# Performance work log

Hardware: AMD Instinct MI355X
Metric: run time of the kernel (lower is better)

## Reference

```python
import jax, jax.numpy as jnp
import numpy as np

K = 10  # knn_graph default neighbors (self excluded)
NEG = 0.2  # LeakyReLU slope


def lrelu(x):
    return jnp.where(x > 0, x, NEG * x)


def conv1x1_1d(x, w):  # x: (B,Ci,N), w: (Co,Ci)
    return jnp.einsum('oi,bin->bon', w, x)


def conv1x1_2d(x, w):  # x: (B,Ci,N,k), w: (Co,Ci)
    return jnp.einsum('oi,bink->bonk', w, x)


def bn1(x, s, b):  # folded eval-mode BN, x: (B,C,N)
    return x * s[None, :, None] + b[None, :, None]


def bn2(x, s, b):  # x: (B,C,N,k)
    return x * s[None, :, None, None] + b[None, :, None, None]


def knn_graph(x, k=K):
    # x: (B, D, N) -> edge features (B, 2D, N, k)
    xt = jnp.transpose(x, (0, 2, 1))  # (B,N,D)
    sq = jnp.sum(xt * xt, axis=-1)  # (B,N)
    d2 = sq[:, :, None] + sq[:, None, :] - 2.0 * jnp.einsum('bnd,bmd->bnm', xt, xt)
    _, idx = jax.lax.top_k(-d2, k + 1)  # nearest k+1 incl. self
    idx = idx[:, :, 1:]  # drop self -> (B,N,k)
    B = xt.shape[0]
    feats = xt[jnp.arange(B)[:, None, None], idx]  # (B,N,k,D)
    center = xt[:, :, None, :]  # (B,N,1,D)
    edge = jnp.concatenate((feats - center, jnp.broadcast_to(center, feats.shape)), axis=-1)
    return jnp.transpose(edge, (0, 3, 1, 2))  # (B,2D,N,k)


def _make_params(key):
    ks = iter(jax.random.split(key, 32))
    def W(co, ci):
        return jax.random.normal(next(ks), (co, ci), jnp.float32) * (1.0 / np.sqrt(ci))
    def SB(c):
        return (jax.random.uniform(next(ks), (c,), jnp.float32, 0.5, 1.5),
                jax.random.normal(next(ks), (c,), jnp.float32) * 0.1)
    p = {}
    p['w1'] = W(64, 6);    p['s1'], p['b1'] = SB(64)
    p['w2'] = W(64, 64);   p['s2'], p['b2'] = SB(64)
    p['w3'] = W(64, 128);  p['s3'], p['b3'] = SB(64)
    p['w4'] = W(64, 64);   p['s4'], p['b4'] = SB(64)
    p['w5'] = W(64, 128);  p['s5'], p['b5'] = SB(64)
    p['w6'] = W(1024, 192); p['s6'], p['b6'] = SB(1024)
    p['w7'] = W(64, 16);   p['s7'], p['b7'] = SB(64)
    p['wp1'] = W(256, 1280); p['sp1'], p['bp1'] = SB(256)
    p['wp2'] = W(256, 256);  p['sp2'], p['bp2'] = SB(256)
    p['wp3'] = W(128, 256);  p['sp3'], p['bp3'] = SB(128)
    p['wp4'] = W(6, 128)
    return p


def setup_inputs() -> dict:
    key = jax.random.key(0)
    k0, k1, k2 = jax.random.split(key, 3)
    inp = {
        'points': jax.random.normal(k0, (8, 2048, 3), jnp.float32),
        'label': jax.random.uniform(k1, (8, 16), jnp.float32),
    }
    inp.update(_make_params(k2))
    return inp


def reference(points, label,
              w1, s1, b1, w2, s2, b2, w3, s3, b3, w4, s4, b4, w5, s5, b5,
              w6, s6, b6, w7, s7, b7,
              wp1, sp1, bp1, wp2, sp2, bp2, wp3, sp3, bp3, wp4):
    B, N, _ = points.shape
    x0 = jnp.transpose(points, (0, 2, 1))  # (B,3,N)

    e1 = knn_graph(x0)                                   # (B,6,N,k)
    h = lrelu(bn2(conv1x1_2d(e1, w1), s1, b1))
    out1 = jnp.max(lrelu(bn2(conv1x1_2d(h, w2), s2, b2)), axis=-1)  # (B,64,N)

    e2 = knn_graph(out1)                                 # (B,128,N,k)
    h = lrelu(bn2(conv1x1_2d(e2, w3), s3, b3))
    out2 = jnp.max(lrelu(bn2(conv1x1_2d(h, w4), s4, b4)), axis=-1)  # (B,64,N)

    e3 = knn_graph(out2)                                 # (B,128,N,k)
    out3 = jnp.max(lrelu(bn2(conv1x1_2d(e3, w5), s5, b5)), axis=-1)  # (B,64,N)

    comb = jnp.concatenate((out1, out2, out3), axis=1)   # (B,192,N)
    out4 = lrelu(bn1(conv1x1_1d(comb, w6), s6, b6))      # (B,1024,N)
    out4 = jnp.max(out4, axis=-1, keepdims=True)         # (B,1024,1)

    cat_vet = lrelu(bn1(conv1x1_1d(label[:, :, None], w7), s7, b7))  # (B,64,1)
    glob = jnp.broadcast_to(jnp.concatenate((out4, cat_vet), axis=1), (B, 1088, N))

    out = jnp.concatenate((out1, out2, out3, glob), axis=1)  # (B,1280,N)
    out = lrelu(bn1(conv1x1_1d(out, wp1), sp1, bp1))
    out = lrelu(bn1(conv1x1_1d(out, wp2), sp2, bp2))  # dropout = identity (eval)
    out = lrelu(bn1(conv1x1_1d(out, wp3), sp3, bp3))
    out = conv1x1_1d(out, wp4)                         # (B,6,N)
    return jnp.transpose(out, (0, 2, 1))               # (B,N,6)
```

## Files before the change

kernel.cpp:

```cpp
#include <hip/hip_runtime.h>
#include <float.h>

#define NEG 0.2f
constexpr int BATCH = 8;
constexpr int NPTS  = 2048;
constexpr int KNN   = 10;
constexpr int KP1   = 11;

__device__ __forceinline__ float lrelu(float x) { return x > 0.f ? x : NEG * x; }

__device__ __forceinline__ unsigned long long dkey(float d, int m) {
    unsigned u = __float_as_uint(d);
    u ^= (unsigned)((int)u >> 31) | 0x80000000u;
    return ((unsigned long long)u << 32) | (unsigned)m;
}

template<int D>
__global__ void sq_kernel(const float* __restrict__ xt, float* __restrict__ sq) {
    int i = blockIdx.x * 256 + threadIdx.x;
    if (i >= BATCH * NPTS) return;
    const float* p = xt + (size_t)i * D;
    float s = 0.f;
    #pragma unroll
    for (int d = 0; d < D; ++d) s += p[d] * p[d];
    sq[i] = s;
}

__global__ void sq64_kernel(const float* __restrict__ xt, float* __restrict__ sq) {
    int i = blockIdx.x * 256 + threadIdx.x;
    if (i >= BATCH * NPTS) return;
    const float4* p = (const float4*)(xt + (size_t)i * 64);
    float4 s4 = {0.f, 0.f, 0.f, 0.f};
    #pragma unroll
    for (int d = 0; d < 16; ++d) {
        float4 v = p[d];
        s4.x += v.x * v.x; s4.y += v.y * v.y; s4.z += v.z * v.z; s4.w += v.w * v.w;
    }
    sq[i] = (s4.x + s4.y) + (s4.z + s4.w);
}

__global__ __launch_bounds__(64) void knn3_kernel(const float* __restrict__ xt,
                                                  const float* __restrict__ sq,
                                                  int* __restrict__ idx_out) {
    const int bn = blockIdx.x;
    const int b  = bn >> 11;
    const int l  = threadIdx.x;

    const float qx = xt[(size_t)bn * 3 + 0];
    const float qy = xt[(size_t)bn * 3 + 1];
    const float qz = xt[(size_t)bn * 3 + 2];
    const float sqn = sq[bn];
    const float* xb  = xt + (size_t)b * NPTS * 3;
    const float* sqb_ = sq + (size_t)b * NPTS;

    unsigned long long lk[KP1];
    #pragma unroll
    for (int j = 0; j < KP1; ++j) lk[j] = ~0ULL;

    for (int m = l; m < NPTS; m += 64) {
        float dot = 0.f;
        dot += qx * xb[m * 3 + 0];
        dot += qy * xb[m * 3 + 1];
        dot += qz * xb[m * 3 + 2];
        float cd = sqn + sqb_[m] - 2.f * dot;
        unsigned long long key = dkey(cd, m);
        if (key < lk[KP1 - 1]) {
            #pragma unroll
            for (int j = 0; j < KP1; ++j) {
                bool better = key < lk[j];
                unsigned long long tk = lk[j];
                if (better) { lk[j] = key; key = tk; }
            }
        }
    }

    #pragma unroll
    for (int k = 0; k < KP1; ++k) {
        unsigned long long mk = lk[0];
        #pragma unroll
        for (int s = 32; s >= 1; s >>= 1) {
            unsigned long long o = __shfl_xor(mk, s, 64);
            mk = (o < mk) ? o : mk;
        }
        if (k >= 1 && l == k - 1)
            idx_out[(size_t)bn * KNN + (k - 1)] = (int)(unsigned)mk;
        if (lk[0] == mk) {
            #pragma unroll
            for (int j = 0; j < KP1 - 1; ++j) lk[j] = lk[j + 1];
            lk[KP1 - 1] = ~0ULL;
        }
    }
}

__global__ __launch_bounds__(256) void knn64_kernel(const float* __restrict__ xt,
                                                    const float* __restrict__ sq,
                                                    int* __restrict__ idx_out) {
    const int t  = threadIdx.x;
    const int qg = t >> 5;
    const int lc = t & 31;
    const int h  = qg & 1;
    const int w  = t >> 6;
    const int bn0 = blockIdx.x * 8;
    const int bn  = bn0 + qg;
    const int qA  = bn0 + 2 * w;
    const int qB  = qA + 1;
    const int b   = bn >> 11;
    const float* xb = xt + (size_t)b * NPTS * 64;

    __shared__ __align__(16) float4 tile4[2][32][16];

    float4 xqa[8], xqb[8];
    {
        const float4* pa = (const float4*)(xt + (size_t)qA * 64 + h * 32);
        const float4* pb = (const float4*)(xt + (size_t)qB * 64 + h * 32);
        #pragma unroll
        for (int i = 0; i < 8; ++i) { xqa[i] = pa[i]; xqb[i] = pb[i]; }
    }
    const float sqn = sq[bn];
    const float* sqb_ = sq + b * NPTS;

    unsigned long long lk[KP1];
    #pragma unroll
    for (int j = 0; j < KP1; ++j) lk[j] = ~0ULL;

    const int ci  = t >> 3;
    const int sub = t & 7;

    int ro[8];
    #pragma unroll
    for (int i = 0; i < 8; ++i) ro[i] = (h * 8 + i) ^ (lc & 15);
    const int wo0 = (2 * sub)     ^ (ci & 15);
    const int wo1 = (2 * sub + 1) ^ (ci & 15);

    const float4* rb0 = &tile4[0][lc][0];
    const float4* rb1 = &tile4[1][lc][0];
    float4*       wb0 = &tile4[0][ci][0];
    float4*       wb1 = &tile4[1][ci][0];

    const float4* src = (const float4*)(xb + (size_t)ci * 64 + sub * 8);

    {
        float4 u0 = src[0], u1 = src[1];
        wb0[wo0] = u0;
        wb0[wo1] = u1;
    }
    __syncthreads();
    src += 512;

    for (int t0 = 0; t0 < NPTS; t0 += 32) {
        float4 n0, n1;
        const bool more = (t0 + 32 < NPTS);
        if (more) { n0 = src[0]; n1 = src[1]; }

        float a0 = 0.f, a1 = 0.f, a2 = 0.f, a3 = 0.f;
        float c0 = 0.f, c1 = 0.f, c2 = 0.f, c3 = 0.f;
        #pragma unroll
        for (int i = 0; i < 8; ++i) {
            float4 v = rb0[ro[i]];
            a0 += xqa[i].x * v.x; a1 += xqa[i].y * v.y;
            a2 += xqa[i].z * v.z; a3 += xqa[i].w * v.w;
            c0 += xqb[i].x * v.x; c1 += xqb[i].y * v.y;
            c2 += xqb[i].z * v.z; c3 += xqb[i].w * v.w;
        }
        float pA = (a0 + a1) + (a2 + a3);
        float pB = (c0 + c1) + (c2 + c3);
        float oA = __shfl_xor(pA, 32, 64);
        float oB = __shfl_xor(pB, 32, 64);
        float dot = (h == 0) ? (pA + oA) : (oB + pB);

        const int m = t0 + lc;
        float cd = sqn + sqb_[m] - 2.f * dot;
        unsigned long long key = dkey(cd, m);
        if (key < lk[KP1 - 1]) {
            #pragma unroll
            for (int j = 0; j < KP1; ++j) {
                bool better = key < lk[j];
                unsigned long long tk = lk[j];
                if (better) { lk[j] = key; key = tk; }
            }
        }

        if (more) {
            wb1[wo0] = n0;
            wb1[wo1] = n1;
        }
        __syncthreads();
        { const float4* tr = rb0; rb0 = rb1; rb1 = tr; }
        { float4* tw = wb0; wb0 = wb1; wb1 = tw; }
        src += 512;
    }

    #pragma unroll
    for (int k = 0; k < KP1; ++k) {
        unsigned long long mk = lk[0];
        #pragma unroll
        for (int s = 16; s >= 1; s >>= 1) {
            unsigned long long o = __shfl_xor(mk, s, 32);
            mk = (o < mk) ? o : mk;
        }
        if (k >= 1 && lc == k - 1)
            idx_out[(size_t)bn * KNN + (k - 1)] = (int)(unsigned)mk;
        if (lk[0] == mk) {
            #pragma unroll
            for (int j = 0; j < KP1 - 1; ++j) lk[j] = lk[j + 1];
            lk[KP1 - 1] = ~0ULL;
        }
    }
}

__global__ __launch_bounds__(64) void edgeconv1_kernel(
    const float* __restrict__ pts, const int* __restrict__ idx,
    const float* __restrict__ w1, const float* __restrict__ s1, const float* __restrict__ b1,
    const float* __restrict__ w2, const float* __restrict__ s2, const float* __restrict__ b2,
    float* __restrict__ outt) {
    const int bn = blockIdx.x;
    const int b  = bn / NPTS;
    const int c  = threadIdx.x;

    const float cx = pts[bn * 3 + 0], cy = pts[bn * 3 + 1], cz = pts[bn * 3 + 2];

    float w1r[6];
    #pragma unroll
    for (int i = 0; i < 6; ++i) w1r[i] = w1[c * 6 + i];
    const float s1c = s1[c], b1c = b1[c], s2c = s2[c], b2c = b2[c];

    __shared__ float h1all[KNN][64];
    #pragma unroll
    for (int k = 0; k < KNN; ++k) {
        const int m = idx[bn * KNN + k];
        const float* f = pts + ((size_t)b * NPTS + m) * 3;
        const float e0 = f[0] - cx, e1 = f[1] - cy, e2 = f[2] - cz;
        float a = w1r[0] * e0 + w1r[1] * e1 + w1r[2] * e2
                + w1r[3] * cx + w1r[4] * cy + w1r[5] * cz;
        h1all[k][c] = lrelu(a * s1c + b1c);
    }
    __syncthreads();

    float a2[KNN];
    #pragma unroll
    for (int k = 0; k < KNN; ++k) a2[k] = 0.f;
    for (int j4 = 0; j4 < 16; ++j4) {
        float4 wv = *(const float4*)&w2[c * 64 + j4 * 4];
        #pragma unroll
        for (int k = 0; k < KNN; ++k) {
            float4 h4 = *(const float4*)&h1all[k][j4 * 4];
            a2[k] += wv.x * h4.x + wv.y * h4.y + wv.z * h4.z + wv.w * h4.w;
        }
    }
    float mx = -FLT_MAX;
    #pragma unroll
    for (int k = 0; k < KNN; ++k) mx = fmaxf(mx, lrelu(a2[k] * s2c + b2c));
    outt[(size_t)bn * 64 + c] = mx;
}

__global__ __launch_bounds__(64) void edgeconv2_kernel(
    const float* __restrict__ xin, const int* __restrict__ idx,
    const float* __restrict__ w3, const float* __restrict__ s3, const float* __restrict__ b3,
    const float* __restrict__ w4, const float* __restrict__ s4, const float* __restrict__ b4,
    float* __restrict__ outt) {
    const int bn = blockIdx.x;
    const int b  = bn / NPTS;
    const int c  = threadIdx.x;

    __shared__ float cen[64];
    __shared__ float fea[KNN][64];
    __shared__ float h1all[KNN][64];
    cen[c] = xin[(size_t)bn * 64 + c];
    #pragma unroll
    for (int k = 0; k < KNN; ++k) {
        const int m = idx[bn * KNN + k];
        fea[k][c] = xin[((size_t)b * NPTS + m) * 64 + c];
    }
    __syncthreads();

    float a[KNN];
    #pragma unroll
    for (int k = 0; k < KNN; ++k) a[k] = 0.f;
    float4 ab = {0.f, 0.f, 0.f, 0.f};
    for (int j4 = 0; j4 < 16; ++j4) {
        float4 wa = *(const float4*)&w3[c * 128 + j4 * 4];
        float4 wb = *(const float4*)&w3[c * 128 + 64 + j4 * 4];
        float4 c4 = *(const float4*)&cen[j4 * 4];
        ab.x += (wb.x - wa.x) * c4.x; ab.y += (wb.y - wa.y) * c4.y;
        ab.z += (wb.z - wa.z) * c4.z; ab.w += (wb.w - wa.w) * c4.w;
        #pragma unroll
        for (int k = 0; k < KNN; ++k) {
            float4 f4 = *(const float4*)&fea[k][j4 * 4];
            a[k] += wa.x * f4.x + wa.y * f4.y + wa.z * f4.z + wa.w * f4.w;
        }
    }
    const float abase = (ab.x + ab.y) + (ab.z + ab.w);
    const float s3c = s3[c], b3c = b3[c], s4c = s4[c], b4c = b4[c];
    #pragma unroll
    for (int k = 0; k < KNN; ++k) h1all[k][c] = lrelu((a[k] + abase) * s3c + b3c);
    __syncthreads();

    float a2[KNN];
    #pragma unroll
    for (int k = 0; k < KNN; ++k) a2[k] = 0.f;
    for (int j4 = 0; j4 < 16; ++j4) {
        float4 wv = *(const float4*)&w4[c * 64 + j4 * 4];
        #pragma unroll
        for (int k = 0; k < KNN; ++k) {
            float4 h4 = *(const float4*)&h1all[k][j4 * 4];
            a2[k] += wv.x * h4.x + wv.y * h4.y + wv.z * h4.z + wv.w * h4.w;
        }
    }
    float mx = -FLT_MAX;
    #pragma unroll
    for (int k = 0; k < KNN; ++k) mx = fmaxf(mx, lrelu(a2[k] * s4c + b4c));
    outt[(size_t)bn * 64 + c] = mx;
}

__global__ __launch_bounds__(64) void edgeconv3_kernel(
    const float* __restrict__ xin, const int* __restrict__ idx,
    const float* __restrict__ w5, const float* __restrict__ s5, const float* __restrict__ b5,
    float* __restrict__ outt) {
    const int bn = blockIdx.x;
    const int b  = bn / NPTS;
    const int c  = threadIdx.x;

    __shared__ float cen[64];
    __shared__ float fea[KNN][64];
    cen[c] = xin[(size_t)bn * 64 + c];
    #pragma unroll
    for (int k = 0; k < KNN; ++k) {
        const int m = idx[bn * KNN + k];
        fea[k][c] = xin[((size_t)b * NPTS + m) * 64 + c];
    }
    __syncthreads();

    float a[KNN];
    #pragma unroll
    for (int k = 0; k < KNN; ++k) a[k] = 0.f;
    float4 ab = {0.f, 0.f, 0.f, 0.f};
    for (int j4 = 0; j4 < 16; ++j4) {
        float4 wa = *(const float4*)&w5[c * 128 + j4 * 4];
        float4 wb = *(const float4*)&w5[c * 128 + 64 + j4 * 4];
        float4 c4 = *(const float4*)&cen[j4 * 4];
        ab.x += (wb.x - wa.x) * c4.x; ab.y += (wb.y - wa.y) * c4.y;
        ab.z += (wb.z - wa.z) * c4.z; ab.w += (wb.w - wa.w) * c4.w;
        #pragma unroll
        for (int k = 0; k < KNN; ++k) {
            float4 f4 = *(const float4*)&fea[k][j4 * 4];
            a[k] += wa.x * f4.x + wa.y * f4.y + wa.z * f4.z + wa.w * f4.w;
        }
    }
    const float abase = (ab.x + ab.y) + (ab.z + ab.w);
    const float s5c = s5[c], b5c = b5[c];
    float mx = -FLT_MAX;
    #pragma unroll
    for (int k = 0; k < KNN; ++k) mx = fmaxf(mx, lrelu((a[k] + abase) * s5c + b5c));
    outt[(size_t)bn * 64 + c] = mx;
}

__global__ __launch_bounds__(64) void catvet_kernel(
    const float* __restrict__ label,
    const float* __restrict__ w7, const float* __restrict__ s7, const float* __restrict__ b7,
    float* __restrict__ catv) {
    const int b = blockIdx.x, c = threadIdx.x;
    float a = 0.f;
    #pragma unroll
    for (int i = 0; i < 16; ++i) a += w7[c * 16 + i] * label[b * 16 + i];
    catv[b * 64 + c] = lrelu(a * s7[c] + b7[c]);
}

__global__ void w6t_kernel(const float* __restrict__ w6, float* __restrict__ w6t) {
    int i = blockIdx.x * 256 + threadIdx.x;
    if (i >= 192 * 1024) return;
    int k = i >> 10, c = i & 1023;
    w6t[i] = w6[c * 192 + k];
}

constexpr int OPTS = 32;
__global__ __launch_bounds__(256) void out4max_kernel(
    const float* __restrict__ out1t, const float* __restrict__ out2t, const float* __restrict__ out3t,
    const float* __restrict__ w6t, float* __restrict__ partial) {
    const int blk = blockIdx.x;
    const int b   = blk >> 6;
    const int nt  = blk & 63;
    const int t   = threadIdx.x;

    __shared__ float xs[192 * OPTS];
    for (int idx = t; idx < 192 * OPTS; idx += 256) {
        int p = idx / 192, r = idx - p * 192;
        const size_t gp = (size_t)b * NPTS + nt * OPTS + p;
        float val;
        if (r < 64)       val = out1t[gp * 64 + r];
        else if (r < 128) val = out2t[gp * 64 + (r - 64)];
        else              val = out3t[gp * 64 + (r - 128)];
        xs[r * OPTS + p] = val;
    }
    __syncthreads();

    float mx0 = -FLT_MAX, mx1 = -FLT_MAX, mx2 = -FLT_MAX, mx3 = -FLT_MAX;
    #pragma unroll
    for (int pg = 0; pg < OPTS / 16; ++pg) {
        float acc0[16], acc1[16], acc2[16], acc3[16];
        #pragma unroll
        for (int p = 0; p < 16; ++p) { acc0[p] = 0.f; acc1[p] = 0.f; acc2[p] = 0.f; acc3[p] = 0.f; }
        #pragma unroll 2
        for (int k = 0; k < 192; ++k) {
            float4 wv = *(const float4*)&w6t[(size_t)k * 1024 + t * 4];
            const float4* xr4 = (const float4*)&xs[k * OPTS + pg * 16];
            #pragma unroll
            for (int p4 = 0; p4 < 4; ++p4) {
                float4 xv = xr4[p4];
                acc0[p4 * 4 + 0] += wv.x * xv.x; acc0[p4 * 4 + 1] += wv.x * xv.y;
                acc0[p4 * 4 + 2] += wv.x * xv.z; acc0[p4 * 4 + 3] += wv.x * xv.w;
                acc1[p4 * 4 + 0] += wv.y * xv.x; acc1[p4 * 4 + 1] += wv.y * xv.y;
                acc1[p4 * 4 + 2] += wv.y * xv.z; acc1[p4 * 4 + 3] += wv.y * xv.w;
                acc2[p4 * 4 + 0] += wv.z * xv.x; acc2[p4 * 4 + 1] += wv.z * xv.y;
                acc2[p4 * 4 + 2] += wv.z * xv.z; acc2[p4 * 4 + 3] += wv.z * xv.w;
                acc3[p4 * 4 + 0] += wv.w * xv.x; acc3[p4 * 4 + 1] += wv.w * xv.y;
                acc3[p4 * 4 + 2] += wv.w * xv.z; acc3[p4 * 4 + 3] += wv.w * xv.w;
            }
        }
        #pragma unroll
        for (int p = 0; p < 16; ++p) {
            mx0 = fmaxf(mx0, acc0[p]); mx1 = fmaxf(mx1, acc1[p]);
            mx2 = fmaxf(mx2, acc2[p]); mx3 = fmaxf(mx3, acc3[p]);
        }
    }
    float4 o = {mx0, mx1, mx2, mx3};
    *(float4*)&partial[(size_t)blk * 1024 + t * 4] = o;
}

__global__ __launch_bounds__(256) void out4reduce_kernel(
    const float* __restrict__ partial,
    const float* __restrict__ s6, const float* __restrict__ b6,
    float* __restrict__ out4m) {
    const int i = blockIdx.x * 256 + threadIdx.x;
    const int b = i >> 10, c = i & 1023;
    float m = -FLT_MAX;
    for (int nt = 0; nt < 64; ++nt)
        m = fmaxf(m, partial[((size_t)b * 64 + nt) * 1024 + c]);
    out4m[i] = lrelu(m * s6[c] + b6[c]);
}

__global__ __launch_bounds__(256) void gbias_kernel(
    const float* __restrict__ out4m, const float* __restrict__ catv,
    const float* __restrict__ wp1, float* __restrict__ g) {
    const int b = blockIdx.x, t = threadIdx.x;
    __shared__ float v[1088];
    for (int i = t; i < 1088; i += 256)
        v[i] = (i < 1024) ? out4m[(size_t)b * 1024 + i] : catv[(size_t)b * 64 + (i - 1024)];
    __syncthreads();
    const float* w = wp1 + (size_t)t * 1280 + 192;
    float4 s4 = {0.f, 0.f, 0.f, 0.f};
    for (int i = 0; i < 272; ++i) {
        float4 wv = *(const float4*)&w[i * 4];
        float4 vv = *(const float4*)&v[i * 4];
        s4.x += wv.x * vv.x; s4.y += wv.y * vv.y; s4.z += wv.z * vv.z; s4.w += wv.w * vv.w;
    }
    g[(size_t)b * 256 + t] = (s4.x + s4.y) + (s4.z + s4.w);
}

constexpr int HP = 16;
constexpr int KC = 16;

__global__ __launch_bounds__(256) void head_kernel(
    const float* __restrict__ out1t, const float* __restrict__ out2t, const float* __restrict__ out3t,
    const float* __restrict__ g,
    const float* __restrict__ wp1, const float* __restrict__ sp1, const float* __restrict__ bp1,
    const float* __restrict__ wp2, const float* __restrict__ sp2, const float* __restrict__ bp2,
    const float* __restrict__ wp3, const float* __restrict__ sp3, const float* __restrict__ bp3,
    const float* __restrict__ wp4, float* __restrict__ out) {
    const int p0 = blockIdx.x * HP;
    const int b  = p0 >> 11;
    const int t  = threadIdx.x;

    __shared__ float smA[4096];
    __shared__ float smB[4096];
    __shared__ float smW[KC * 256];

    for (int e = t; e < 192 * HP; e += 256) {
        int p = e / 192, k = e - p * 192;
        float val;
        if (k < 64)       val = out1t[((size_t)(p0 + p)) * 64 + k];
        else if (k < 128) val = out2t[((size_t)(p0 + p)) * 64 + (k - 64)];
        else              val = out3t[((size_t)(p0 + p)) * 64 + (k - 128)];
        smA[k * HP + p] = val;
    }

    const int og = t & 31;
    const int pg = t >> 5;

    float acc[2][8];
    #pragma unroll
    for (int i = 0; i < 8; ++i) {
        float gv = g[(size_t)b * 256 + og * 8 + i];
        acc[0][i] = gv; acc[1][i] = gv;
    }
    for (int kc = 0; kc < 192 / KC; ++kc) {
        __syncthreads();
        #pragma unroll
        for (int it = 0; it < KC; ++it)
            smW[it * 256 + t] = wp1[(size_t)t * 1280 + kc * KC + it];
        __syncthreads();
        #pragma unroll 4
        for (int kk = 0; kk < KC; ++kk) {
            int k = kc * KC + kk;
            float2 xv = *(const float2*)&smA[k * HP + pg * 2];
            float4 w0 = *(const float4*)&smW[kk * 256 + og * 8];
            float4 w1v = *(const float4*)&smW[kk * 256 + og * 8 + 4];
            float wv[8] = {w0.x, w0.y, w0.z, w0.w, w1v.x, w1v.y, w1v.z, w1v.w};
            #pragma unroll
            for (int i = 0; i < 8; ++i) {
                acc[0][i] += xv.x * wv[i];
                acc[1][i] += xv.y * wv[i];
            }
        }
    }
    #pragma unroll
    for (int i = 0; i < 8; ++i) {
        int o = og * 8 + i;
        float sc = sp1[o], bc = bp1[o];
        smB[o * HP + pg * 2 + 0] = lrelu(acc[0][i] * sc + bc);
        smB[o * HP + pg * 2 + 1] = lrelu(acc[1][i] * sc + bc);
    }

    float acc2[2][8];
    #pragma unroll
    for (int i = 0; i < 8; ++i) { acc2[0][i] = 0.f; acc2[1][i] = 0.f; }
    for (int kc = 0; kc < 256 / KC; ++kc) {
        __syncthreads();
        #pragma unroll
        for (int it = 0; it < KC; ++it)
            smW[it * 256 + t] = wp2[(size_t)t * 256 + kc * KC + it];
        __syncthreads();
        #pragma unroll 4
        for (int kk = 0; kk < KC; ++kk) {
            int k = kc * KC + kk;
            float2 xv = *(const float2*)&smB[k * HP + pg * 2];
            float4 w0 = *(const float4*)&smW[kk * 256 + og * 8];
            float4 w1v = *(const float4*)&smW[kk * 256 + og * 8 + 4];
            float wv[8] = {w0.x, w0.y, w0.z, w0.w, w1v.x, w1v.y, w1v.z, w1v.w};
            #pragma unroll
            for (int i = 0; i < 8; ++i) {
                acc2[0][i] += xv.x * wv[i];
                acc2[1][i] += xv.y * wv[i];
            }
        }
    }
    __syncthreads();
    #pragma unroll
    for (int i = 0; i < 8; ++i) {
        int o = og * 8 + i;
        float sc = sp2[o], bc = bp2[o];
        smA[o * HP + pg * 2 + 0] = lrelu(acc2[0][i] * sc + bc);
        smA[o * HP + pg * 2 + 1] = lrelu(acc2[1][i] * sc + bc);
    }

    const int og3 = t & 15;
    const int p3  = t >> 4;
    float acc3[8];
    #pragma unroll
    for (int i = 0; i < 8; ++i) acc3[i] = 0.f;
    for (int kc = 0; kc < 256 / KC; ++kc) {
        __syncthreads();
        for (int e = t; e < KC * 128; e += 256) {
            int kk = e >> 7, o = e & 127;
            smW[kk * 128 + o] = wp3[(size_t)o * 256 + kc * KC + kk];
        }
        __syncthreads();
        #pragma unroll 4
        for (int kk = 0; kk < KC; ++kk) {
            int k = kc * KC + kk;
            float xv = smA[k * HP + p3];
            float4 w0 = *(const float4*)&smW[kk * 128 + og3 * 8];
            float4 w1v = *(const float4*)&smW[kk * 128 + og3 * 8 + 4];
            float wv[8] = {w0.x, w0.y, w0.z, w0.w, w1v.x, w1v.y, w1v.z, w1v.w};
            #pragma unroll
            for (int i = 0; i < 8; ++i) acc3[i] += xv * wv[i];
        }
    }
    __syncthreads();
    #pragma unroll
    for (int i = 0; i < 8; ++i) {
        int o = og3 * 8 + i;
        float sc = sp3[o], bc = bp3[o];
        smB[o * HP + p3] = lrelu(acc3[i] * sc + bc);
    }
    __syncthreads();

    if (t < HP * 6) {
        int p = t / 6, o = t - p * 6;
        float4 s4 = {0.f, 0.f, 0.f, 0.f};
        for (int k4 = 0; k4 < 32; ++k4) {
            float4 wv = *(const float4*)&wp4[o * 128 + k4 * 4];
            s4.x += wv.x * smB[(k4 * 4 + 0) * HP + p];
            s4.y += wv.y * smB[(k4 * 4 + 1) * HP + p];
            s4.z += wv.z * smB[(k4 * 4 + 2) * HP + p];
            s4.w += wv.w * smB[(k4 * 4 + 3) * HP + p];
        }
        out[((size_t)(p0 + p)) * 6 + o] = (s4.x + s4.y) + (s4.z + s4.w);
    }
}

extern "C" void kernel_launch(void* const* d_in, const int* in_sizes, int n_in,
                              void* d_out, int out_size, void* d_ws, size_t ws_size,
                              hipStream_t stream) {
    const float* points = (const float*)d_in[0];
    const float* label  = (const float*)d_in[1];
    const float* w1  = (const float*)d_in[2];
    const float* s1  = (const float*)d_in[3];
    const float* b1  = (const float*)d_in[4];
    const float* w2  = (const float*)d_in[5];
    const float* s2  = (const float*)d_in[6];
    const float* b2  = (const float*)d_in[7];
    const float* w3  = (const float*)d_in[8];
    const float* s3  = (const float*)d_in[9];
    const float* b3  = (const float*)d_in[10];
    const float* w4  = (const float*)d_in[11];
    const float* s4  = (const float*)d_in[12];
    const float* b4  = (const float*)d_in[13];
    const float* w5  = (const float*)d_in[14];
    const float* s5  = (const float*)d_in[15];
    const float* b5  = (const float*)d_in[16];
    const float* w6  = (const float*)d_in[17];
    const float* s6  = (const float*)d_in[18];
    const float* b6  = (const float*)d_in[19];
    const float* w7  = (const float*)d_in[20];
    const float* s7  = (const float*)d_in[21];
    const float* b7  = (const float*)d_in[22];
    const float* wp1 = (const float*)d_in[23];
    const float* sp1 = (const float*)d_in[24];
    const float* bp1 = (const float*)d_in[25];
    const float* wp2 = (const float*)d_in[26];
    const float* sp2 = (const float*)d_in[27];
    const float* bp2 = (const float*)d_in[28];
    const float* wp3 = (const float*)d_in[29];
    const float* sp3 = (const float*)d_in[30];
    const float* bp3 = (const float*)d_in[31];
    const float* wp4 = (const float*)d_in[32];

    float* ws = (float*)d_ws;
    size_t off = 0;
    auto alloc = [&](size_t nf) { float* p = ws + off; off += nf; return p; };
    float* out1t = alloc((size_t)BATCH * NPTS * 64);
    float* out2t = alloc((size_t)BATCH * NPTS * 64);
    float* out3t = alloc((size_t)BATCH * NPTS * 64);
    float* sqb   = alloc((size_t)BATCH * NPTS);
    float* out4m = alloc((size_t)BATCH * 1024);
    float* catv  = alloc((size_t)BATCH * 64);
    float* gb    = alloc((size_t)BATCH * 256);
    float* w6t   = alloc((size_t)192 * 1024);
    float* part  = alloc((size_t)512 * 1024);
    int* idx1 = (int*)alloc((size_t)BATCH * NPTS * KNN);
    int* idx2 = (int*)alloc((size_t)BATCH * NPTS * KNN);
    int* idx3 = (int*)alloc((size_t)BATCH * NPTS * KNN);

    const int BN = BATCH * NPTS;
    const int sqBlocks = (BN + 255) / 256;

    sq_kernel<3><<<sqBlocks, 256, 0, stream>>>(points, sqb);
    knn3_kernel<<<BN, 64, 0, stream>>>(points, sqb, idx1);
    edgeconv1_kernel<<<BN, 64, 0, stream>>>(points, idx1, w1, s1, b1, w2, s2, b2, out1t);

    sq64_kernel<<<sqBlocks, 256, 0, stream>>>(out1t, sqb);
    knn64_kernel<<<BN / 8, 256, 0, stream>>>(out1t, sqb, idx2);
    edgeconv2_kernel<<<BN, 64, 0, stream>>>(out1t, idx2, w3, s3, b3, w4, s4, b4, out2t);

    sq64_kernel<<<sqBlocks, 256, 0, stream>>>(out2t, sqb);
    knn64_kernel<<<BN / 8, 256, 0, stream>>>(out2t, sqb, idx3);
    edgeconv3_kernel<<<BN, 64, 0, stream>>>(out2t, idx3, w5, s5, b5, out3t);

    catvet_kernel<<<BATCH, 64, 0, stream>>>(label, w7, s7, b7, catv);
    w6t_kernel<<<(192 * 1024 + 255) / 256, 256, 0, stream>>>(w6, w6t);
    out4max_kernel<<<512, 256, 0, stream>>>(out1t, out2t, out3t, w6t, part);
    out4reduce_kernel<<<BATCH * 1024 / 256, 256, 0, stream>>>(part, s6, b6, out4m);
    gbias_kernel<<<BATCH, 256, 0, stream>>>(out4m, catv, wp1, gb);

    head_kernel<<<BN / HP, 256, 0, stream>>>(out1t, out2t, out3t, gb,
                                             wp1, sp1, bp1, wp2, sp2, bp2, wp3, sp3, bp3,
                                             wp4, (float*)d_out);
}
```

Before: 1.092 ms.

## Process eight points per block in edgeconv kernels with two channels per thread

The three edge-convolution kernels now handle 8 points per 256-thread block instead of one point per 64-thread block. Each thread computes two output channels, so every weight float4 load feeds two channel accumulators and there are far fewer blocks to launch. Neighbour indices and features are staged cooperatively in shared memory. In exchange, each thread holds twice as many accumulators (more register pressure), and each block uses more shared memory, which may reduce occupancy.

After: 1.099 ms. Within noise of the previous version (+0.7%).

```diff
diff --git a/kernel.cpp b/kernel.cpp
--- a/kernel.cpp
+++ b/kernel.cpp
@@ -208,150 +208,214 @@
     }
 }
 
-__global__ __launch_bounds__(64) void edgeconv1_kernel(
+__global__ __launch_bounds__(256) void edgeconv1_kernel(
     const float* __restrict__ pts, const int* __restrict__ idx,
     const float* __restrict__ w1, const float* __restrict__ s1, const float* __restrict__ b1,
     const float* __restrict__ w2, const float* __restrict__ s2, const float* __restrict__ b2,
     float* __restrict__ outt) {
-    const int bn = blockIdx.x;
-    const int b  = bn / NPTS;
-    const int c  = threadIdx.x;
-
-    const float cx = pts[bn * 3 + 0], cy = pts[bn * 3 + 1], cz = pts[bn * 3 + 2];
-
-    float w1r[6];
-    #pragma unroll
-    for (int i = 0; i < 6; ++i) w1r[i] = w1[c * 6 + i];
-    const float s1c = s1[c], b1c = b1[c], s2c = s2[c], b2c = b2[c];
-
-    __shared__ float h1all[KNN][64];
+    const int p0g = blockIdx.x * 8;
+    const int b   = p0g >> 11;
+    const int t   = threadIdx.x;
+    const int p   = t >> 5;
+    const int c32 = t & 31;
+    const int pn  = p0g + p;
+    const int c0 = c32, c1 = c32 + 32;
+
+    __shared__ int   sidx[8][KNN];
+    __shared__ float h1s[8][KNN][64];
+
+    if (t < 8 * KNN) sidx[t / KNN][t % KNN] = idx[(size_t)(p0g + t / KNN) * KNN + (t % KNN)];
+    __syncthreads();
+
+    const float cx = pts[pn * 3 + 0], cy = pts[pn * 3 + 1], cz = pts[pn * 3 + 2];
+    float w1r0[6], w1r1[6];
+    #pragma unroll
+    for (int i = 0; i < 6; ++i) { w1r0[i] = w1[c0 * 6 + i]; w1r1[i] = w1[c1 * 6 + i]; }
+    const float s1c0 = s1[c0], b1c0 = b1[c0], s1c1 = s1[c1], b1c1 = b1[c1];
+
     #pragma unroll
     for (int k = 0; k < KNN; ++k) {
-        const int m = idx[bn * KNN + k];
+        const int m = sidx[p][k];
         const float* f = pts + ((size_t)b * NPTS + m) * 3;
         const float e0 = f[0] - cx, e1 = f[1] - cy, e2 = f[2] - cz;
-        float a = w1r[0] * e0 + w1r[1] * e1 + w1r[2] * e2
-                + w1r[3] * cx + w1r[4] * cy + w1r[5] * cz;
-        h1all[k][c] = lrelu(a * s1c + b1c);
-    }
-    __syncthreads();
-
-    float a2[KNN];
-    #pragma unroll
-    for (int k = 0; k < KNN; ++k) a2[k] = 0.f;
+        float a0 = w1r0[0] * e0 + w1r0[1] * e1 + w1r0[2] * e2
+                 + w1r0[3] * cx + w1r0[4] * cy + w1r0[5] * cz;
+        float a1 = w1r1[0] * e0 + w1r1[1] * e1 + w1r1[2] * e2
+                 + w1r1[3] * cx + w1r1[4] * cy + w1r1[5] * cz;
+        h1s[p][k][c0] = lrelu(a0 * s1c0 + b1c0);
+        h1s[p][k][c1] = lrelu(a1 * s1c1 + b1c1);
+    }
+    __syncthreads();
+
+    float a20[KNN], a21[KNN];
+    #pragma unroll
+    for (int k = 0; k < KNN; ++k) { a20[k] = 0.f; a21[k] = 0.f; }
     for (int j4 = 0; j4 < 16; ++j4) {
-        float4 wv = *(const float4*)&w2[c * 64 + j4 * 4];
+        float4 wv0 = *(const float4*)&w2[c0 * 64 + j4 * 4];
+        float4 wv1 = *(const float4*)&w2[c1 * 64 + j4 * 4];
         #pragma unroll
         for (int k = 0; k < KNN; ++k) {
-            float4 h4 = *(const float4*)&h1all[k][j4 * 4];
-            a2[k] += wv.x * h4.x + wv.y * h4.y + wv.z * h4.z + wv.w * h4.w;
-        }
-    }
-    float mx = -FLT_MAX;
-    #pragma unroll
-    for (int k = 0; k < KNN; ++k) mx = fmaxf(mx, lrelu(a2[k] * s2c + b2c));
-    outt[(size_t)bn * 64 + c] = mx;
-}
-
-__global__ __launch_bounds__(64) void edgeconv2_kernel(
+            float4 h4 = *(const float4*)&h1s[p][k][j4 * 4];
+            a20[k] += wv0.x * h4.x + wv0.y * h4.y + wv0.z * h4.z + wv0.w * h4.w;
+            a21[k] += wv1.x * h4.x + wv1.y * h4.y + wv1.z * h4.z + wv1.w * h4.w;
+        }
+    }
+    const float s2c0 = s2[c0], b2c0 = b2[c0], s2c1 = s2[c1], b2c1 = b2[c1];
+    float mx0 = -FLT_MAX, mx1 = -FLT_MAX;
+    #pragma unroll
+    for (int k = 0; k < KNN; ++k) {
+        mx0 = fmaxf(mx0, lrelu(a20[k] * s2c0 + b2c0));
+        mx1 = fmaxf(mx1, lrelu(a21[k] * s2c1 + b2c1));
+    }
+    outt[(size_t)pn * 64 + c0] = mx0;
+    outt[(size_t)pn * 64 + c1] = mx1;
+}
+
+__global__ __launch_bounds__(256) void edgeconv2_kernel(
     const float* __restrict__ xin, const int* __restrict__ idx,
     const float* __restrict__ w3, const float* __restrict__ s3, const float* __restrict__ b3,
     const float* __restrict__ w4, const float* __restrict__ s4, const float* __restrict__ b4,
     float* __restrict__ outt) {
-    const int bn = blockIdx.x;
-    const int b  = bn / NPTS;
-    const int c  = threadIdx.x;
-
-    __shared__ float cen[64];
-    __shared__ float fea[KNN][64];
-    __shared__ float h1all[KNN][64];
-    cen[c] = xin[(size_t)bn * 64 + c];
+    const int p0g = blockIdx.x * 8;
+    const int b   = p0g >> 11;
+    const int t   = threadIdx.x;
+    const int p   = t >> 5;
+    const int c32 = t & 31;
+    const int pn  = p0g + p;
+    const int c0 = c32, c1 = c32 + 32;
+
+    __shared__ int   sidx[8][KNN];
+    __shared__ float cens[8][64];
+    __shared__ float feas[8][KNN][64];
+    __shared__ float h1s[8][KNN][64];
+
+    if (t < 8 * KNN) sidx[t / KNN][t % KNN] = idx[(size_t)(p0g + t / KNN) * KNN + (t % KNN)];
+    for (int i = t; i < 8 * 64; i += 256)
+        cens[i >> 6][i & 63] = xin[((size_t)p0g + (i >> 6)) * 64 + (i & 63)];
+    __syncthreads();
+    for (int i = t; i < 8 * KNN * 64; i += 256) {
+        int pp = i / (KNN * 64), r = i - pp * (KNN * 64);
+        int k = r >> 6, c = r & 63;
+        feas[pp][k][c] = xin[((size_t)b * NPTS + sidx[pp][k]) * 64 + c];
+    }
+    __syncthreads();
+
+    float a0[KNN], a1[KNN];
+    #pragma unroll
+    for (int k = 0; k < KNN; ++k) { a0[k] = 0.f; a1[k] = 0.f; }
+    float4 ab0 = {0.f, 0.f, 0.f, 0.f};
+    float4 ab1 = {0.f, 0.f, 0.f, 0.f};
+    for (int j4 = 0; j4 < 16; ++j4) {
+        float4 wa0 = *(const float4*)&w3[c0 * 128 + j4 * 4];
+        float4 wb0 = *(const float4*)&w3[c0 * 128 + 64 + j4 * 4];
+        float4 wa1 = *(const float4*)&w3[c1 * 128 + j4 * 4];
+        float4 wb1 = *(const float4*)&w3[c1 * 128 + 64 + j4 * 4];
+        float4 c4 = *(const float4*)&cens[p][j4 * 4];
+        ab0.x += (wb0.x - wa0.x) * c4.x; ab0.y += (wb0.y - wa0.y) * c4.y;
+        ab0.z += (wb0.z - wa0.z) * c4.z; ab0.w += (wb0.w - wa0.w) * c4.w;
+        ab1.x += (wb1.x - wa1.x) * c4.x; ab1.y += (wb1.y - wa1.y) * c4.y;
+        ab1.z += (wb1.z - wa1.z) * c4.z; ab1.w += (wb1.w - wa1.w) * c4.w;
+        #pragma unroll
+        for (int k = 0; k < KNN; ++k) {
+            float4 f4 = *(const float4*)&feas[p][k][j4 * 4];
+            a0[k] += wa0.x * f4.x + wa0.y * f4.y + wa0.z * f4.z + wa0.w * f4.w;
+            a1[k] += wa1.x * f4.x + wa1.y * f4.y + wa1.z * f4.z + wa1.w * f4.w;
+        }
+    }
+    const float abase0 = (ab0.x + ab0.y) + (ab0.z + ab0.w);
+    const float abase1 = (ab1.x + ab1.y) + (ab1.z + ab1.w);
+    const float s3c0 = s3[c0], b3c0 = b3[c0], s3c1 = s3[c1], b3c1 = b3[c1];
     #pragma unroll
     for (int k = 0; k < KNN; ++k) {
-        const int m = idx[bn * KNN + k];
-        fea[k][c] = xin[((size_t)b * NPTS + m) * 64 + c];
-    }
-    __syncthreads();
-
-    float a[KNN];
-    #pragma unroll
-    for (int k = 0; k < KNN; ++k) a[k] = 0.f;
-    float4 ab = {0.f, 0.f, 0.f, 0.f};
+        h1s[p][k][c0] = lrelu((a0[k] + abase0) * s3c0 + b3c0);
+        h1s[p][k][c1] = lrelu((a1[k] + abase1) * s3c1 + b3c1);
+    }
+    __syncthreads();
+
+    float a20[KNN], a21[KNN];
+    #pragma unroll
+    for (int k = 0; k < KNN; ++k) { a20[k] = 0.f; a21[k] = 0.f; }
     for (int j4 = 0; j4 < 16; ++j4) {
-        float4 wa = *(const float4*)&w3[c * 128 + j4 * 4];
-        float4 wb = *(const float4*)&w3[c * 128 + 64 + j4 * 4];
-        float4 c4 = *(const float4*)&cen[j4 * 4];
-        ab.x += (wb.x - wa.x) * c4.x; ab.y += (wb.y - wa.y) * c4.y;
-        ab.z += (wb.z - wa.z) * c4.z; ab.w += (wb.w - wa.w) * c4.w;
+        float4 wv0 = *(const float4*)&w4[c0 * 64 + j4 * 4];
+        float4 wv1 = *(const float4*)&w4[c1 * 64 + j4 * 4];
         #pragma unroll
         for (int k = 0; k < KNN; ++k) {
-            float4 f4 = *(const float4*)&fea[k][j4 * 4];
-            a[k] += wa.x * f4.x + wa.y * f4.y + wa.z * f4.z + wa.w * f4.w;
-        }
-    }
-    const float abase = (ab.x + ab.y) + (ab.z + ab.w);
-    const float s3c = s3[c], b3c = b3[c], s4c = s4[c], b4c = b4[c];
-    #pragma unroll
-    for (int k = 0; k < KNN; ++k) h1all[k][c] = lrelu((a[k] + abase) * s3c + b3c);
-    __syncthreads();
-
-    float a2[KNN];
-    #pragma unroll
-    for (int k = 0; k < KNN; ++k) a2[k] = 0.f;
-    for (int j4 = 0; j4 < 16; ++j4) {
-        float4 wv = *(const float4*)&w4[c * 64 + j4 * 4];
-        #pragma unroll
-        for (int k = 0; k < KNN; ++k) {
-            float4 h4 = *(const float4*)&h1all[k][j4 * 4];
-            a2[k] += wv.x * h4.x + wv.y * h4.y + wv.z * h4.z + wv.w * h4.w;
-        }
-    }
-    float mx = -FLT_MAX;
-    #pragma unroll
-    for (int k = 0; k < KNN; ++k) mx = fmaxf(mx, lrelu(a2[k] * s4c + b4c));
-    outt[(size_t)bn * 64 + c] = mx;
-}
-
-__global__ __launch_bounds__(64) void edgeconv3_kernel(
+            float4 h4 = *(const float4*)&h1s[p][k][j4 * 4];
+            a20[k] += wv0.x * h4.x + wv0.y * h4.y + wv0.z * h4.z + wv0.w * h4.w;
+            a21[k] += wv1.x * h4.x + wv1.y * h4.y + wv1.z * h4.z + wv1.w * h4.w;
+        }
+    }
+    const float s4c0 = s4[c0], b4c0 = b4[c0], s4c1 = s4[c1], b4c1 = b4[c1];
+    float mx0 = -FLT_MAX, mx1 = -FLT_MAX;
+    #pragma unroll
+    for (int k = 0; k < KNN; ++k) {
+        mx0 = fmaxf(mx0, lrelu(a20[k] * s4c0 + b4c0));
+        mx1 = fmaxf(mx1, lrelu(a21[k] * s4c1 + b4c1));
+    }
+    outt[(size_t)pn * 64 + c0] = mx0;
+    outt[(size_t)pn * 64 + c1] = mx1;
+}
+
+__global__ __launch_bounds__(256) void edgeconv3_kernel(
     const float* __restrict__ xin, const int* __restrict__ idx,
     const float* __restrict__ w5, const float* __restrict__ s5, const float* __restrict__ b5,
     float* __restrict__ outt) {
-    const int bn = blockIdx.x;
-    const int b  = bn / NPTS;
-    const int c  = threadIdx.x;
-
-    __shared__ float cen[64];
-    __shared__ float fea[KNN][64];
-    cen[c] = xin[(size_t)bn * 64 + c];
+    const int p0g = blockIdx.x * 8;
+    const int b   = p0g >> 11;
+    const int t   = threadIdx.x;
+    const int p   = t >> 5;
+    const int c32 = t & 31;
+    const int pn  = p0g + p;
+    const int c0 = c32, c1 = c32 + 32;
+
+    __shared__ int   sidx[8][KNN];
+    __shared__ float cens[8][64];
+    __shared__ float feas[8][KNN][64];
+
+    if (t < 8 * KNN) sidx[t / KNN][t % KNN] = idx[(size_t)(p0g + t / KNN) * KNN + (t % KNN)];
+    for (int i = t; i < 8 * 64; i += 256)
+        cens[i >> 6][i & 63] = xin[((size_t)p0g + (i >> 6)) * 64 + (i & 63)];
+    __syncthreads();
+    for (int i = t; i < 8 * KNN * 64; i += 256) {
+        int pp = i / (KNN * 64), r = i - pp * (KNN * 64);
+        int k = r >> 6, c = r & 63;
+        feas[pp][k][c] = xin[((size_t)b * NPTS + sidx[pp][k]) * 64 + c];
+    }
+    __syncthreads();
+
+    float a0[KNN], a1[KNN];
+    #pragma unroll
+    for (int k = 0; k < KNN; ++k) { a0[k] = 0.f; a1[k] = 0.f; }
+    float4 ab0 = {0.f, 0.f, 0.f, 0.f};
+    float4 ab1 = {0.f, 0.f, 0.f, 0.f};
+    for (int j4 = 0; j4 < 16; ++j4) {
+        float4 wa0 = *(const float4*)&w5[c0 * 128 + j4 * 4];
+        float4 wb0 = *(const float4*)&w5[c0 * 128 + 64 + j4 * 4];
+        float4 wa1 = *(const float4*)&w5[c1 * 128 + j4 * 4];
+        float4 wb1 = *(const float4*)&w5[c1 * 128 + 64 + j4 * 4];
+        float4 c4 = *(const float4*)&cens[p][j4 * 4];
+        ab0.x += (wb0.x - wa0.x) * c4.x; ab0.y += (wb0.y - wa0.y) * c4.y;
+        ab0.z += (wb0.z - wa0.z) * c4.z; ab0.w += (wb0.w - wa0.w) * c4.w;
+        ab1.x += (wb1.x - wa1.x) * c4.x; ab1.y += (wb1.y - wa1.y) * c4.y;
+        ab1.z += (wb1.z - wa1.z) * c4.z; ab1.w += (wb1.w - wa1.w) * c4.w;
+        #pragma unroll
+        for (int k = 0; k < KNN; ++k) {
+            float4 f4 = *(const float4*)&feas[p][k][j4 * 4];
+            a0[k] += wa0.x * f4.x + wa0.y * f4.y + wa0.z * f4.z + wa0.w * f4.w;
+            a1[k] += wa1.x * f4.x + wa1.y * f4.y + wa1.z * f4.z + wa1.w * f4.w;
+        }
+    }
+    const float abase0 = (ab0.x + ab0.y) + (ab0.z + ab0.w);
+    const float abase1 = (ab1.x + ab1.y) + (ab1.z + ab1.w);
+    const float s5c0 = s5[c0], b5c0 = b5[c0], s5c1 = s5[c1], b5c1 = b5[c1];
+    float mx0 = -FLT_MAX, mx1 = -FLT_MAX;
     #pragma unroll
     for (int k = 0; k < KNN; ++k) {
-        const int m = idx[bn * KNN + k];
-        fea[k][c] = xin[((size_t)b * NPTS + m) * 64 + c];
-    }
-    __syncthreads();
-
-    float a[KNN];
-    #pragma unroll
-    for (int k = 0; k < KNN; ++k) a[k] = 0.f;
-    float4 ab = {0.f, 0.f, 0.f, 0.f};
-    for (int j4 = 0; j4 < 16; ++j4) {
-        float4 wa = *(const float4*)&w5[c * 128 + j4 * 4];
-        float4 wb = *(const float4*)&w5[c * 128 + 64 + j4 * 4];
-        float4 c4 = *(const float4*)&cen[j4 * 4];
-        ab.x += (wb.x - wa.x) * c4.x; ab.y += (wb.y - wa.y) * c4.y;
-        ab.z += (wb.z - wa.z) * c4.z; ab.w += (wb.w - wa.w) * c4.w;
-        #pragma unroll
-        for (int k = 0; k < KNN; ++k) {
-            float4 f4 = *(const float4*)&fea[k][j4 * 4];
-            a[k] += wa.x * f4.x + wa.y * f4.y + wa.z * f4.z + wa.w * f4.w;
-        }
-    }
-    const float abase = (ab.x + ab.y) + (ab.z + ab.w);
-    const float s5c = s5[c], b5c = b5[c];
-    float mx = -FLT_MAX;
-    #pragma unroll
-    for (int k = 0; k < KNN; ++k) mx = fmaxf(mx, lrelu((a[k] + abase) * s5c + b5c));
-    outt[(size_t)bn * 64 + c] = mx;
+        mx0 = fmaxf(mx0, lrelu((a0[k] + abase0) * s5c0 + b5c0));
+        mx1 = fmaxf(mx1, lrelu((a1[k] + abase1) * s5c1 + b5c1));
+    }
+    outt[(size_t)pn * 64 + c0] = mx0;
+    outt[(size_t)pn * 64 + c1] = mx1;
 }
 
 __global__ __launch_bounds__(64) void catvet_kernel(
@@ -656,15 +720,15 @@
 
     sq_kernel<3><<<sqBlocks, 256, 0, stream>>>(points, sqb);
     knn3_kernel<<<BN, 64, 0, stream>>>(points, sqb, idx1);
-    edgeconv1_kernel<<<BN, 64, 0, stream>>>(points, idx1, w1, s1, b1, w2, s2, b2, out1t);
+    edgeconv1_kernel<<<BN / 8, 256, 0, stream>>>(points, idx1, w1, s1, b1, w2, s2, b2, out1t);
 
     sq64_kernel<<<sqBlocks, 256, 0, stream>>>(out1t, sqb);
     knn64_kernel<<<BN / 8, 256, 0, stream>>>(out1t, sqb, idx2);
-    edgeconv2_kernel<<<BN, 64, 0, stream>>>(out1t, idx2, w3, s3, b3, w4, s4, b4, out2t);
+    edgeconv2_kernel<<<BN / 8, 256, 0, stream>>>(out1t, idx2, w3, s3, b3, w4, s4, b4, out2t);
 
     sq64_kernel<<<sqBlocks, 256, 0, stream>>>(out2t, sqb);
     knn64_kernel<<<BN / 8, 256, 0, stream>>>(out2t, sqb, idx3);
-    edgeconv3_kernel<<<BN, 64, 0, stream>>>(out2t, idx3, w5, s5, b5, out3t);
+    edgeconv3_kernel<<<BN / 8, 256, 0, stream>>>(out2t, idx3, w5, s5, b5, out3t);
 
     catvet_kernel<<<BATCH, 64, 0, stream>>>(label, w7, s7, b7, catv);
     w6t_kernel<<<(192 * 1024 + 255) / 256, 256, 0, stream>>>(w6, w6t);
```
